# Optimization experiments

Measured on AMD Instinct MI355X. Metric: run time of the kernel, lower is better.

## Reference

```python
import jax, jax.numpy as jnp
import numpy as np
from jax import lax

H, H2, VJ, VC = 512, 256, 70, 2000
B, LIN, T = 64, 1024, 256
START = 1  # char2index['<s>']


def gru_step(h, x, Wih, Whh, bih, bhh):
    # PyTorch GRU cell math; gates ordered (r, z, n)
    gi = x @ Wih.T + bih
    gh = h @ Whh.T + bhh
    ir, iz, inn = jnp.split(gi, 3, axis=-1)
    hr, hz, hn = jnp.split(gh, 3, axis=-1)
    r = jax.nn.sigmoid(ir + hr)
    z = jax.nn.sigmoid(iz + hz)
    n = jnp.tanh(inn + r * hn)
    return (1.0 - z) * n + z * h


def setup_inputs() -> dict:
    key = jax.random.key(0)
    ks = jax.random.split(key, 24)
    u = lambda k, s: jax.random.uniform(k, s, jnp.float32, -0.1, 0.1)
    return {
        "input_tokens": jax.random.randint(ks[0], (B, LIN), 0, VJ),
        "target_tokens": jax.random.randint(ks[1], (B, T), 0, VC),
        "loss_mask": jnp.ones((B, T), jnp.float32),
        "emb_jamo": u(ks[2], (VJ, H)),
        "emb_char": u(ks[3], (VC, H)),
        "enc_Wih_f": u(ks[4], (3 * H2, H)),  "enc_Whh_f": u(ks[5], (3 * H2, H2)),
        "enc_bih_f": u(ks[6], (3 * H2,)),    "enc_bhh_f": u(ks[7], (3 * H2,)),
        "enc_Wih_b": u(ks[8], (3 * H2, H)),  "enc_Whh_b": u(ks[9], (3 * H2, H2)),
        "enc_bih_b": u(ks[10], (3 * H2,)),   "enc_bhh_b": u(ks[11], (3 * H2,)),
        "dec_Wih": u(ks[12], (3 * H, H)),    "dec_Whh": u(ks[13], (3 * H, H)),
        "dec_bih": u(ks[14], (3 * H,)),      "dec_bhh": u(ks[15], (3 * H,)),
        "attn_W": u(ks[16], (H, 2 * H)),     "attn_b": u(ks[17], (H,)),
        "comb_W": u(ks[18], (H, 2 * H)),     "comb_b": u(ks[19], (H,)),
        "out_W": u(ks[20], (VC, H)),         "out_b": u(ks[21], (VC,)),
    }


def reference(input_tokens, target_tokens, loss_mask, emb_jamo, emb_char,
              enc_Wih_f, enc_Whh_f, enc_bih_f, enc_bhh_f,
              enc_Wih_b, enc_Whh_b, enc_bih_b, enc_bhh_b,
              dec_Wih, dec_Whh, dec_bih, dec_bhh,
              attn_W, attn_b, comb_W, comb_b, out_W, out_b):
    b, lin = input_tokens.shape
    t_len = target_tokens.shape[1]
    h2 = enc_Whh_f.shape[1]

    # --- Encoder: step-by-step bidirectional GRU (per original Python loop,
    # both directions advance forward in time since seq_len=1 per call) ---
    xs = jnp.swapaxes(emb_jamo[input_tokens], 0, 1)  # [Lin, B, H]

    def enc_step(carry, xt):
        hf, hb = carry
        hf = gru_step(hf, xt, enc_Wih_f, enc_Whh_f, enc_bih_f, enc_bhh_f)
        hb = gru_step(hb, xt, enc_Wih_b, enc_Whh_b, enc_bih_b, enc_bhh_b)
        return (hf, hb), jnp.concatenate([hf, hb], axis=-1)

    init = (jnp.zeros((b, h2), xs.dtype), jnp.zeros((b, h2), xs.dtype))
    _, enc_out_t = lax.scan(enc_step, init, xs)      # [Lin, B, H]
    enc_out = jnp.swapaxes(enc_out_t, 0, 1)          # [B, Lin, H]
    h0 = enc_out_t[-1]                               # decoder init hidden [B, H]

    # --- Decoder: attention + GRU, greedy argmax feedback ---
    tok0 = jnp.full((b,), START, dtype=input_tokens.dtype)

    def dec_step(carry, _):
        tok, h = carry
        emb = emb_char[tok]                                           # [B, H]
        key_ = jnp.concatenate([emb, h], -1) @ attn_W.T + attn_b      # [B, H]
        scores = jnp.einsum('blh,bh->bl', enc_out, key_)              # [B, Lin]
        w = jax.nn.softmax(scores, axis=1)
        ctx = jnp.einsum('bl,blh->bh', w, enc_out)                    # [B, H]
        g = jax.nn.relu(jnp.concatenate([emb, ctx], -1) @ comb_W.T + comb_b)
        h_new = gru_step(h, g, dec_Wih, dec_Whh, dec_bih, dec_bhh)
        logp = jax.nn.log_softmax(h_new @ out_W.T + out_b, axis=-1)   # [B, VC]
        nxt = jnp.argmax(logp, axis=-1).astype(tok.dtype)
        return (nxt, h_new), (logp, w)

    _, (logps, ws) = lax.scan(dec_step, (tok0, h0), None, length=t_len)
    decoder_outputs = jnp.swapaxes(logps, 0, 1)       # [B, T, VC]
    decoder_attentions = jnp.transpose(ws, (1, 2, 0)) # [B, Lin, T]

    # NLLLoss(reduction='none') masked, mean over batch, summed over steps, /T
    nll = -jnp.take_along_axis(decoder_outputs, target_tokens[..., None], axis=-1)[..., 0]
    loss = jnp.sum(jnp.mean(nll * loss_mask, axis=0)) / t_len
    return decoder_outputs, decoder_attentions, loss
```

## Files before the change

kernel.cpp:

```cpp
#include <hip/hip_runtime.h>
#include <hip/hip_bf16.h>
#include <cstdint>
#include <cstddef>


#define DEV __device__ __forceinline__

constexpr int kH = 512, kH2 = 256, kVC = 2000, kB = 64, kLIN = 1024, kT = 256;
constexpr int kSTART = 1;

__global__ __launch_bounds__(256) void k_zero(float* p, int n) {
  int i = blockIdx.x * 256 + threadIdx.x;
  if (i < n) p[i] = 0.f;
}

__global__ __launch_bounds__(256)
void k_gi_table(const float* emb_jamo, const float* Wf, const float* Wb,
                const float* bihf, const float* bihb, float* gi) {
  int v = blockIdx.x >> 1, d = blockIdx.x & 1;
  const float* W = d ? Wb : Wf;
  const float* bih = d ? bihb : bihf;
  __shared__ float x[kH];
  for (int k = threadIdx.x; k < kH; k += 256) x[k] = emb_jamo[v * kH + k];
  __syncthreads();
  for (int j = threadIdx.x; j < 3 * kH2; j += 256) {
    float acc = bih[j];
    const float* row = W + (size_t)j * kH;
    for (int k = 0; k < kH; k += 4) {
      float4 f = *(const float4*)(row + k);
      acc += x[k] * f.x + x[k + 1] * f.y + x[k + 2] * f.z + x[k + 3] * f.w;
    }
    gi[(size_t)(v * 2 + d) * 768 + j] = acc;
  }
}

__global__ __launch_bounds__(256)
void k_ac_emb(const float* emb_char, const float* attn_W, const float* attn_b,
              const float* comb_W, const float* comb_b, float* A, float* C) {
  int v = blockIdx.x;
  __shared__ float x[kH];
  for (int k = threadIdx.x; k < kH; k += 256) x[k] = emb_char[v * kH + k];
  __syncthreads();
  for (int j = threadIdx.x; j < kH; j += 256) {
    float a = attn_b[j], c = comb_b[j];
    const float* ra = attn_W + (size_t)j * 1024;
    const float* rc = comb_W + (size_t)j * 1024;
    for (int k = 0; k < kH; k += 4) {
      float4 fa = *(const float4*)(ra + k), fc = *(const float4*)(rc + k);
      a += x[k] * fa.x + x[k + 1] * fa.y + x[k + 2] * fa.z + x[k + 3] * fa.w;
      c += x[k] * fc.x + x[k + 1] * fc.y + x[k + 2] * fc.z + x[k + 3] * fc.w;
    }
    A[(size_t)v * kH + j] = a;
    C[(size_t)v * kH + j] = c;
  }
}

__global__ __launch_bounds__(256)
void k_enc_step(const int* tokens, const float* Whf, const float* Whb,
                const float* bhhf, const float* bhhb, const float* gi,
                float* henc, float* enc, int t, int pp, int BC, int lbc, int b0) {
  int d = blockIdx.x >> lbc;
  int blk = blockIdx.x & (BC - 1);
  int b = threadIdx.x & (BC - 1), q = threadIdx.x >> lbc;
  int u = blk * (256 >> lbc) + q;
  const float* Whh = d ? Whb : Whf;
  const float* bhh = d ? bhhb : bhhf;
  const float* hin = henc + (size_t)(pp * 2 + d) * kH2 * BC;
  float* hout = henc + (size_t)((1 - pp) * 2 + d) * kH2 * BC;

  const float* wr = Whh + (size_t)(0 * kH2 + u) * kH2;
  const float* wz = Whh + (size_t)(1 * kH2 + u) * kH2;
  const float* wn = Whh + (size_t)(2 * kH2 + u) * kH2;
  float ar = bhh[u], az = bhh[kH2 + u], an = bhh[2 * kH2 + u];
  for (int k = 0; k < kH2; k += 4) {
    float4 fr = *(const float4*)(wr + k);
    float4 fz = *(const float4*)(wz + k);
    float4 fn = *(const float4*)(wn + k);
    float h0v = hin[(k + 0) * BC + b], h1v = hin[(k + 1) * BC + b];
    float h2v = hin[(k + 2) * BC + b], h3v = hin[(k + 3) * BC + b];
    ar += h0v * fr.x + h1v * fr.y + h2v * fr.z + h3v * fr.w;
    az += h0v * fz.x + h1v * fz.y + h2v * fz.z + h3v * fz.w;
    an += h0v * fn.x + h1v * fn.y + h2v * fn.z + h3v * fn.w;
  }
  int v = tokens[(size_t)(b0 + b) * kLIN + t];
  const float* git = gi + (size_t)(v * 2 + d) * 768;
  float r = 1.f / (1.f + expf(-(git[u] + ar)));
  float z = 1.f / (1.f + expf(-(git[kH2 + u] + az)));
  float n = tanhf(git[2 * kH2 + u] + r * an);
  float hprev = hin[u * BC + b];
  float hnew = (1.f - z) * n + z * hprev;
  hout[u * BC + b] = hnew;
  enc[((size_t)b * kLIN + t) * kH + d * kH2 + u] = hnew;
}

__global__ __launch_bounds__(256)
void k_prologue(const float* enc, const float* Atab, const float* aW,
                float* hr, float* ht, float* key, int* tok, int BC) {
  int b = blockIdx.x, tid = threadIdx.x;
  __shared__ float h[kH];
  const float* h0 = enc + ((size_t)b * kLIN + (kLIN - 1)) * kH;
  for (int k = tid; k < kH; k += 256) {
    float v = h0[k];
    h[k] = v;
    hr[(size_t)b * kH + k] = v;
    ht[(size_t)k * BC + b] = v;
  }
  if (tid == 0) tok[b] = kSTART;
  __syncthreads();
  const float* A = Atab + (size_t)kSTART * kH;
  for (int j = tid; j < kH; j += 256) {
    const float* row = aW + (size_t)j * 1024 + 512;
    float acc = A[j];
    for (int k = 0; k < kH; k += 4) {
      float4 f = *(const float4*)(row + k);
      acc += h[k] * f.x + h[k + 1] * f.y + h[k + 2] * f.z + h[k + 3] * f.w;
    }
    key[(size_t)b * kH + j] = acc;
  }
}

__global__ __launch_bounds__(256)
void k_scores(const float* encAll, const float* keyAll, float* sc,
              float* pm, float* pd, float* pctx) {
  int b = blockIdx.x >> 3, lt = blockIdx.x & 7;
  int tid = threadIdx.x, lane = tid & 63, w = tid >> 6, hl = lane & 31, half = lane >> 5;
  __shared__ float s_tile[128], e_tile[128], red[128];
  const float* enc = encAll + (size_t)b * kLIN * kH;
  float kreg[16];
  const float* key = keyAll + (size_t)b * kH + hl * 16;
#pragma unroll
  for (int m = 0; m < 16; m += 4) *(float4*)(kreg + m) = *(const float4*)(key + m);
  for (int i = 0; i < 16; i++) {
    int ll = w * 32 + i * 2 + half;
    int l = lt * 128 + ll;
    const float* row = enc + (size_t)l * kH + hl * 16;
    float acc = 0.f;
#pragma unroll
    for (int m = 0; m < 16; m += 4) {
      float4 v = *(const float4*)(row + m);
      acc += v.x * kreg[m] + v.y * kreg[m + 1] + v.z * kreg[m + 2] + v.w * kreg[m + 3];
    }
#pragma unroll
    for (int m2 = 16; m2 > 0; m2 >>= 1) acc += __shfl_xor(acc, m2, 32);
    if (hl == 0) { s_tile[ll] = acc; sc[(size_t)b * kLIN + l] = acc; }
  }
  __syncthreads();
  if (tid < 128) red[tid] = s_tile[tid];
  __syncthreads();
  for (int s = 64; s > 0; s >>= 1) {
    if (tid < s) red[tid] = fmaxf(red[tid], red[tid + s]);
    __syncthreads();
  }
  float mt = red[0];
  __syncthreads();
  if (tid < 128) { e_tile[tid] = expf(s_tile[tid] - mt); red[tid] = e_tile[tid]; }
  __syncthreads();
  for (int s = 64; s > 0; s >>= 1) {
    if (tid < s) red[tid] += red[tid + s];
    __syncthreads();
  }
  float dt = red[0];
  int h0i = tid * 2;
  float cx = 0.f, cy = 0.f;
  const float* base = enc + (size_t)(lt * 128) * kH + h0i;
  for (int l = 0; l < 128; l++) {
    float e = e_tile[l];
    float2 v = *(const float2*)(base + (size_t)l * kH);
    cx += e * v.x; cy += e * v.y;
  }
  float* pc = pctx + ((size_t)b * 8 + lt) * kH;
  pc[h0i] = cx; pc[h0i + 1] = cy;
  if (tid == 0) { pm[b * 8 + lt] = mt; pd[b * 8 + lt] = dt; }
}

__global__ __launch_bounds__(256)
void k_ctx_g(const float* cW, const float* Ctab, const float* sc,
             const float* pm, const float* pd, const float* pctx,
             const int* tok, float* out1, float* gt, int BC, int b0, int t) {
  int b = blockIdx.x, tid = threadIdx.x;
  __shared__ float f8[8], MD[2], ctxl[kH];
  __shared__ int tokl;
  if (tid == 0) {
    float M = -1e30f;
    for (int i = 0; i < 8; i++) M = fmaxf(M, pm[b * 8 + i]);
    float D = 0.f;
    for (int i = 0; i < 8; i++) {
      float f = expf(pm[b * 8 + i] - M);
      f8[i] = f; D += f * pd[b * 8 + i];
    }
    MD[0] = M; MD[1] = 1.f / D;
    tokl = tok[b];
  }
  __syncthreads();
  float M = MD[0], invD = MD[1];
  int h0i = tid * 2;
  float cx = 0.f, cy = 0.f;
  for (int i = 0; i < 8; i++) {
    const float* pc = pctx + ((size_t)b * 8 + i) * kH + h0i;
    cx += f8[i] * pc[0]; cy += f8[i] * pc[1];
  }
  ctxl[h0i] = cx * invD; ctxl[h0i + 1] = cy * invD;
  int gb = b0 + b;
  for (int l = tid; l < kLIN; l += 256)
    out1[((size_t)gb * kLIN + l) * kT + t] = expf(sc[(size_t)b * kLIN + l] - M) * invD;
  __syncthreads();
  int tk = tokl;
  for (int j = tid; j < kH; j += 256) {
    const float* row = cW + (size_t)j * 1024 + 512;
    float acc = Ctab[(size_t)tk * kH + j];
    for (int k = 0; k < kH; k += 4) {
      float4 f = *(const float4*)(row + k);
      acc += ctxl[k] * f.x + ctxl[k + 1] * f.y + ctxl[k + 2] * f.z + ctxl[k + 3] * f.w;
    }
    gt[(size_t)j * BC + b] = fmaxf(acc, 0.f);
  }
}

__global__ __launch_bounds__(256)
void k_gru(const float* Wih, const float* Whh, const float* bih, const float* bhh,
           const float* gt, float* ht, float* hr, int BC, int lbc, int pp) {
  int tid = threadIdx.x;
  int b = tid & (BC - 1), q = tid >> lbc;
  int u = blockIdx.x * (256 >> lbc) + q;
  const float* htp = ht + (size_t)pp * kH * BC;
  float air = bih[u], aiz = bih[kH + u], ain = bih[2 * kH + u];
  float ahr = bhh[u], ahz = bhh[kH + u], ahn = bhh[2 * kH + u];
  const float* wir = Wih + (size_t)(0 * kH + u) * kH;
  const float* wiz = Wih + (size_t)(1 * kH + u) * kH;
  const float* win = Wih + (size_t)(2 * kH + u) * kH;
  const float* whr = Whh + (size_t)(0 * kH + u) * kH;
  const float* whz = Whh + (size_t)(1 * kH + u) * kH;
  const float* whn = Whh + (size_t)(2 * kH + u) * kH;
  for (int k = 0; k < kH; k += 4) {
    float4 fir = *(const float4*)(wir + k), fiz = *(const float4*)(wiz + k), fin = *(const float4*)(win + k);
    float4 fhr = *(const float4*)(whr + k), fhz = *(const float4*)(whz + k), fhn = *(const float4*)(whn + k);
    float g0 = gt[(k + 0) * BC + b], g1 = gt[(k + 1) * BC + b];
    float g2 = gt[(k + 2) * BC + b], g3 = gt[(k + 3) * BC + b];
    float h0v = htp[(k + 0) * BC + b], h1v = htp[(k + 1) * BC + b];
    float h2v = htp[(k + 2) * BC + b], h3v = htp[(k + 3) * BC + b];
    air += g0 * fir.x + g1 * fir.y + g2 * fir.z + g3 * fir.w;
    aiz += g0 * fiz.x + g1 * fiz.y + g2 * fiz.z + g3 * fiz.w;
    ain += g0 * fin.x + g1 * fin.y + g2 * fin.z + g3 * fin.w;
    ahr += h0v * fhr.x + h1v * fhr.y + h2v * fhr.z + h3v * fhr.w;
    ahz += h0v * fhz.x + h1v * fhz.y + h2v * fhz.z + h3v * fhz.w;
    ahn += h0v * fhn.x + h1v * fhn.y + h2v * fhn.z + h3v * fhn.w;
  }
  float r = 1.f / (1.f + expf(-(air + ahr)));
  float z = 1.f / (1.f + expf(-(aiz + ahz)));
  float n = tanhf(ain + r * ahn);
  float hp = htp[(size_t)u * BC + b];
  float hnew = (1.f - z) * n + z * hp;
  ht[(size_t)(1 - pp) * kH * BC + (size_t)u * BC + b] = hnew;
  hr[(size_t)(1 - pp) * BC * kH + (size_t)b * kH + u] = hnew;
}

__global__ __launch_bounds__(256)
void k_logits(const float* oW, const float* ob, const float* hr, float* lg,
              int BC, int np) {
  int b = blockIdx.x >> 3, ct = blockIdx.x & 7;
  int tid = threadIdx.x, lane = tid & 63, w = tid >> 6, hl = lane & 31, half = lane >> 5;
  const float* hrow = hr + (size_t)np * BC * kH + (size_t)b * kH + hl * 16;
  float hreg[16];
#pragma unroll
  for (int m = 0; m < 16; m += 4) *(float4*)(hreg + m) = *(const float4*)(hrow + m);
  int c0 = ct * 250;
  for (int i = 0; i < 32; i++) {
    int c = c0 + i * 8 + w * 2 + half;
    if (c < c0 + 250) {
      const float* row = oW + (size_t)c * kH + hl * 16;
      float acc = 0.f;
#pragma unroll
      for (int m = 0; m < 16; m += 4) {
        float4 v = *(const float4*)(row + m);
        acc += v.x * hreg[m] + v.y * hreg[m + 1] + v.z * hreg[m + 2] + v.w * hreg[m + 3];
      }
#pragma unroll
      for (int m2 = 16; m2 > 0; m2 >>= 1) acc += __shfl_xor(acc, m2, 32);
      if (hl == 0) lg[(size_t)b * kVC + c] = acc + ob[c];
    }
  }
}

__global__ __launch_bounds__(256)
void k_finish(const float* aW, const int* targets, const float* mask,
              const float* Atab, const float* hr, const float* lg,
              float* key, int* tok, float* loss, float* out0,
              int BC, int b0, int t, int np) {
  int b = blockIdx.x, tid = threadIdx.x, gb = b0 + b;
  __shared__ float rv[256]; __shared__ int ri[256]; __shared__ float rs[256];
  __shared__ float hsh[kH];
  const float* lrow = lg + (size_t)b * kVC;
  float xv[8];
  float bv = -3.4e38f; int bi = kVC;
#pragma unroll
  for (int i = 0; i < 8; i++) {
    int c = tid + i * 256;
    float x = (c < kVC) ? lrow[c] : -3.4e38f;
    xv[i] = x;
    if (x > bv) { bv = x; bi = c; }
  }
  rv[tid] = bv; ri[tid] = bi;
  __syncthreads();
  for (int s = 128; s > 0; s >>= 1) {
    if (tid < s) {
      float v2 = rv[tid + s]; int i2 = ri[tid + s];
      if (v2 > rv[tid] || (v2 == rv[tid] && i2 < ri[tid])) { rv[tid] = v2; ri[tid] = i2; }
    }
    __syncthreads();
  }
  float M = rv[0]; int nt = ri[0];
  float se = 0.f;
#pragma unroll
  for (int i = 0; i < 8; i++) { int c = tid + i * 256; if (c < kVC) se += expf(xv[i] - M); }
  rs[tid] = se;
  __syncthreads();
  for (int s = 128; s > 0; s >>= 1) {
    if (tid < s) rs[tid] += rs[tid + s];
    __syncthreads();
  }
  float lse = M + logf(rs[0]);
  float* orow = out0 + ((size_t)gb * kT + t) * kVC;
#pragma unroll
  for (int i = 0; i < 8; i++) { int c = tid + i * 256; if (c < kVC) orow[c] = xv[i] - lse; }
  if (tid == 0) {
    tok[b] = nt;
    int tg = targets[(size_t)gb * kT + t];
    float mk = mask[(size_t)gb * kT + t];
    atomicAdd(loss, (lse - lrow[tg]) * mk * (1.f / 16384.f));
  }
  const float* hrow = hr + (size_t)np * BC * kH + (size_t)b * kH;
  for (int k = tid; k < kH; k += 256) hsh[k] = hrow[k];
  __syncthreads();
  const float* A = Atab + (size_t)nt * kH;
  for (int j = tid; j < kH; j += 256) {
    const float* row = aW + (size_t)j * 1024 + 512;
    float acc = A[j];
    for (int k = 0; k < kH; k += 4) {
      float4 f = *(const float4*)(row + k);
      acc += hsh[k] * f.x + hsh[k + 1] * f.y + hsh[k + 2] * f.z + hsh[k + 3] * f.w;
    }
    key[(size_t)b * kH + j] = acc;
  }
}

__global__ void k_loss_out(float* dst, const float* loss) {
  if (threadIdx.x == 0 && blockIdx.x == 0) *dst = *loss;
}

extern "C" void kernel_launch(void* const* d_in, const int* in_sizes, int n_in,
                              void* d_out, int out_size, void* d_ws, size_t ws_size,
                              hipStream_t stream) {
  (void)in_sizes; (void)n_in;
  const int*   tok_in = (const int*)d_in[0];
  const int*   tgt    = (const int*)d_in[1];
  const float* mask   = (const float*)d_in[2];
  const float* emb_j  = (const float*)d_in[3];
  const float* emb_c  = (const float*)d_in[4];
  const float* eWif   = (const float*)d_in[5];
  const float* eWhf   = (const float*)d_in[6];
  const float* ebif   = (const float*)d_in[7];
  const float* ebhf   = (const float*)d_in[8];
  const float* eWib   = (const float*)d_in[9];
  const float* eWhb   = (const float*)d_in[10];
  const float* ebib   = (const float*)d_in[11];
  const float* ebhb   = (const float*)d_in[12];
  const float* dWi    = (const float*)d_in[13];
  const float* dWh    = (const float*)d_in[14];
  const float* dbi    = (const float*)d_in[15];
  const float* dbh    = (const float*)d_in[16];
  const float* aW     = (const float*)d_in[17];
  const float* ab     = (const float*)d_in[18];
  const float* cW     = (const float*)d_in[19];
  const float* cb     = (const float*)d_in[20];
  const float* oW     = (const float*)d_in[21];
  const float* ob     = (const float*)d_in[22];
  float* ws   = (float*)d_ws;
  float* out0 = (float*)d_out;
  float* out1 = out0 + (size_t)kB * kT * kVC;

  const size_t GI = 0;
  const size_t A  = GI + 107520;
  const size_t C  = A + 1024000;
  const size_t SMALL = C + 1024000;
  size_t o = SMALL;
  const size_t HENC = o; o += 4 * 256 * 64;
  const size_t KEY  = o; o += 64 * 512;
  const size_t SC   = o; o += 64 * 1024;
  const size_t PM   = o; o += 512;
  const size_t PD   = o; o += 512;
  const size_t PCT  = o; o += 64 * 8 * 512;
  const size_t GT   = o; o += 512 * 64;
  const size_t HR   = o; o += 2 * 64 * 512;
  const size_t HT   = o; o += 2 * 512 * 64;
  const size_t LG   = o; o += 64 * 2000;
  const size_t TOKo = o; o += 64;
  const size_t LOSS = o; o += 1;
  const size_t ENC  = o;
  const int small_n = (int)(ENC - SMALL);

  int BC = 64;
  while (BC > 8 && (ENC + (size_t)BC * kLIN * kH) * sizeof(float) > ws_size) BC >>= 1;
  int lbc = (BC == 64) ? 6 : (BC == 32) ? 5 : (BC == 16) ? 4 : 3;
  int NC = kB / BC;
  int* tokp = (int*)(ws + TOKo);

  k_zero<<<(small_n + 255) / 256, 256, 0, stream>>>(ws + SMALL, small_n);
  k_gi_table<<<140, 256, 0, stream>>>(emb_j, eWif, eWib, ebif, ebib, ws + GI);
  k_ac_emb<<<2000, 256, 0, stream>>>(emb_c, aW, ab, cW, cb, ws + A, ws + C);

  for (int c = 0; c < NC; c++) {
    int b0 = c * BC;
    k_zero<<<(4 * 256 * BC + 255) / 256, 256, 0, stream>>>(ws + HENC, 4 * 256 * BC);
    for (int t = 0; t < kLIN; t++)
      k_enc_step<<<2 * BC, 256, 0, stream>>>(tok_in, eWhf, eWhb, ebhf, ebhb,
                                             ws + GI, ws + HENC, ws + ENC,
                                             t, t & 1, BC, lbc, b0);
    k_prologue<<<BC, 256, 0, stream>>>(ws + ENC, ws + A, aW, ws + HR, ws + HT,
                                       ws + KEY, tokp, BC);
    for (int t = 0; t < kT; t++) {
      int pp = t & 1, np = 1 - pp;
      k_scores<<<BC * 8, 256, 0, stream>>>(ws + ENC, ws + KEY, ws + SC,
                                           ws + PM, ws + PD, ws + PCT);
      k_ctx_g<<<BC, 256, 0, stream>>>(cW, ws + C, ws + SC, ws + PM, ws + PD,
                                      ws + PCT, tokp, out1, ws + GT, BC, b0, t);
      k_gru<<<2 * BC, 256, 0, stream>>>(dWi, dWh, dbi, dbh, ws + GT,
                                        ws + HT, ws + HR, BC, lbc, pp);
      k_logits<<<BC * 8, 256, 0, stream>>>(oW, ob, ws + HR, ws + LG, BC, np);
      k_finish<<<BC, 256, 0, stream>>>(aW, tgt, mask, ws + A, ws + HR, ws + LG,
                                       ws + KEY, tokp, ws + LOSS, out0,
                                       BC, b0, t, np);
    }
  }
  k_loss_out<<<1, 64, 0, stream>>>(out0 + (size_t)out_size - 1, ws + LOSS);
}
```

Before: 62.72 ms.

## Replace per-step kernel launches with cooperative persistent encoder and decoder kernels

The encoder's 1024 per-timestep launches become one cooperative kernel that loops over time with grid.sync, caching each block's recurrent weight slice in LDS. The decoder's five launches per step are fused into one persistent cooperative kernel whose phases are separated by grid-wide barriers. The aim is to remove kernel launch overhead and weight reloads across thousands of tiny sequential launches. In exchange it relies on grid barrier cost and cooperative-launch support, and keeps the old launch sequence as a fallback if that launch fails.

```diff
diff --git a/kernel.cpp b/kernel.cpp
--- a/kernel.cpp
+++ b/kernel.cpp
@@ -1,10 +1,10 @@
 #include <hip/hip_runtime.h>
-#include <hip/hip_bf16.h>
+#include <hip/hip_cooperative_groups.h>
 #include <cstdint>
 #include <cstddef>
 
-
-#define DEV __device__ __forceinline__
+namespace cg = cooperative_groups;
+
 
 constexpr int kH = 512, kH2 = 256, kVC = 2000, kB = 64, kLIN = 1024, kT = 256;
 constexpr int kSTART = 1;
@@ -55,75 +55,11 @@
   }
 }
 
-__global__ __launch_bounds__(256)
-void k_enc_step(const int* tokens, const float* Whf, const float* Whb,
-                const float* bhhf, const float* bhhb, const float* gi,
-                float* henc, float* enc, int t, int pp, int BC, int lbc, int b0) {
-  int d = blockIdx.x >> lbc;
-  int blk = blockIdx.x & (BC - 1);
-  int b = threadIdx.x & (BC - 1), q = threadIdx.x >> lbc;
-  int u = blk * (256 >> lbc) + q;
-  const float* Whh = d ? Whb : Whf;
-  const float* bhh = d ? bhhb : bhhf;
-  const float* hin = henc + (size_t)(pp * 2 + d) * kH2 * BC;
-  float* hout = henc + (size_t)((1 - pp) * 2 + d) * kH2 * BC;
-
-  const float* wr = Whh + (size_t)(0 * kH2 + u) * kH2;
-  const float* wz = Whh + (size_t)(1 * kH2 + u) * kH2;
-  const float* wn = Whh + (size_t)(2 * kH2 + u) * kH2;
-  float ar = bhh[u], az = bhh[kH2 + u], an = bhh[2 * kH2 + u];
-  for (int k = 0; k < kH2; k += 4) {
-    float4 fr = *(const float4*)(wr + k);
-    float4 fz = *(const float4*)(wz + k);
-    float4 fn = *(const float4*)(wn + k);
-    float h0v = hin[(k + 0) * BC + b], h1v = hin[(k + 1) * BC + b];
-    float h2v = hin[(k + 2) * BC + b], h3v = hin[(k + 3) * BC + b];
-    ar += h0v * fr.x + h1v * fr.y + h2v * fr.z + h3v * fr.w;
-    az += h0v * fz.x + h1v * fz.y + h2v * fz.z + h3v * fz.w;
-    an += h0v * fn.x + h1v * fn.y + h2v * fn.z + h3v * fn.w;
-  }
-  int v = tokens[(size_t)(b0 + b) * kLIN + t];
-  const float* git = gi + (size_t)(v * 2 + d) * 768;
-  float r = 1.f / (1.f + expf(-(git[u] + ar)));
-  float z = 1.f / (1.f + expf(-(git[kH2 + u] + az)));
-  float n = tanhf(git[2 * kH2 + u] + r * an);
-  float hprev = hin[u * BC + b];
-  float hnew = (1.f - z) * n + z * hprev;
-  hout[u * BC + b] = hnew;
-  enc[((size_t)b * kLIN + t) * kH + d * kH2 + u] = hnew;
-}
-
-__global__ __launch_bounds__(256)
-void k_prologue(const float* enc, const float* Atab, const float* aW,
-                float* hr, float* ht, float* key, int* tok, int BC) {
-  int b = blockIdx.x, tid = threadIdx.x;
-  __shared__ float h[kH];
-  const float* h0 = enc + ((size_t)b * kLIN + (kLIN - 1)) * kH;
-  for (int k = tid; k < kH; k += 256) {
-    float v = h0[k];
-    h[k] = v;
-    hr[(size_t)b * kH + k] = v;
-    ht[(size_t)k * BC + b] = v;
-  }
-  if (tid == 0) tok[b] = kSTART;
-  __syncthreads();
-  const float* A = Atab + (size_t)kSTART * kH;
-  for (int j = tid; j < kH; j += 256) {
-    const float* row = aW + (size_t)j * 1024 + 512;
-    float acc = A[j];
-    for (int k = 0; k < kH; k += 4) {
-      float4 f = *(const float4*)(row + k);
-      acc += h[k] * f.x + h[k + 1] * f.y + h[k + 2] * f.z + h[k + 3] * f.w;
-    }
-    key[(size_t)b * kH + j] = acc;
-  }
-}
-
-__global__ __launch_bounds__(256)
-void k_scores(const float* encAll, const float* keyAll, float* sc,
-              float* pm, float* pd, float* pctx) {
-  int b = blockIdx.x >> 3, lt = blockIdx.x & 7;
-  int tid = threadIdx.x, lane = tid & 63, w = tid >> 6, hl = lane & 31, half = lane >> 5;
+
+__device__ void phaseA(int b, int lt, int tid, const float* encAll,
+                       const float* keyAll, float* sc, float* pm, float* pd,
+                       float* pctx) {
+  int lane = tid & 63, w = tid >> 6, hl = lane & 31, half = lane >> 5;
   __shared__ float s_tile[128], e_tile[128], red[128];
   const float* enc = encAll + (size_t)b * kLIN * kH;
   float kreg[16];
@@ -171,13 +107,13 @@
   float* pc = pctx + ((size_t)b * 8 + lt) * kH;
   pc[h0i] = cx; pc[h0i + 1] = cy;
   if (tid == 0) { pm[b * 8 + lt] = mt; pd[b * 8 + lt] = dt; }
-}
-
-__global__ __launch_bounds__(256)
-void k_ctx_g(const float* cW, const float* Ctab, const float* sc,
-             const float* pm, const float* pd, const float* pctx,
-             const int* tok, float* out1, float* gt, int BC, int b0, int t) {
-  int b = blockIdx.x, tid = threadIdx.x;
+  __syncthreads();
+}
+
+__device__ void phaseB(int b, int tid, const float* cW, const float* Ctab,
+                       const float* sc, const float* pm, const float* pd,
+                       const float* pctx, const int* tok, float* out1,
+                       float* gt, int BC, int b0, int t) {
   __shared__ float f8[8], MD[2], ctxl[kH];
   __shared__ int tokl;
   if (tid == 0) {
@@ -214,14 +150,14 @@
     }
     gt[(size_t)j * BC + b] = fmaxf(acc, 0.f);
   }
-}
-
-__global__ __launch_bounds__(256)
-void k_gru(const float* Wih, const float* Whh, const float* bih, const float* bhh,
-           const float* gt, float* ht, float* hr, int BC, int lbc, int pp) {
-  int tid = threadIdx.x;
+  __syncthreads();
+}
+
+__device__ void phaseC(int blk, int tid, const float* Wih, const float* Whh,
+                       const float* bih, const float* bhh, const float* gt,
+                       float* ht, float* hr, int BC, int lbc, int pp) {
   int b = tid & (BC - 1), q = tid >> lbc;
-  int u = blockIdx.x * (256 >> lbc) + q;
+  int u = blk * (256 >> lbc) + q;
   const float* htp = ht + (size_t)pp * kH * BC;
   float air = bih[u], aiz = bih[kH + u], ain = bih[2 * kH + u];
   float ahr = bhh[u], ahz = bhh[kH + u], ahn = bhh[2 * kH + u];
@@ -254,11 +190,9 @@
   hr[(size_t)(1 - pp) * BC * kH + (size_t)b * kH + u] = hnew;
 }
 
-__global__ __launch_bounds__(256)
-void k_logits(const float* oW, const float* ob, const float* hr, float* lg,
-              int BC, int np) {
-  int b = blockIdx.x >> 3, ct = blockIdx.x & 7;
-  int tid = threadIdx.x, lane = tid & 63, w = tid >> 6, hl = lane & 31, half = lane >> 5;
+__device__ void phaseD(int b, int ct, int tid, const float* oW, const float* ob,
+                       const float* hr, float* lg, int BC, int np) {
+  int lane = tid & 63, w = tid >> 6, hl = lane & 31, half = lane >> 5;
   const float* hrow = hr + (size_t)np * BC * kH + (size_t)b * kH + hl * 16;
   float hreg[16];
 #pragma unroll
@@ -281,12 +215,11 @@
   }
 }
 
-__global__ __launch_bounds__(256)
-void k_finish(const float* aW, const int* targets, const float* mask,
-              const float* Atab, const float* hr, const float* lg,
-              float* key, int* tok, float* loss, float* out0,
-              int BC, int b0, int t, int np) {
-  int b = blockIdx.x, tid = threadIdx.x, gb = b0 + b;
+__device__ void phaseE(int b, int tid, const float* aW, const int* targets,
+                       const float* mask, const float* Atab, const float* hr,
+                       const float* lg, float* key, int* tok, float* loss,
+                       float* out0, int BC, int b0, int t, int np) {
+  int gb = b0 + b;
   __shared__ float rv[256]; __shared__ int ri[256]; __shared__ float rs[256];
   __shared__ float hsh[kH];
   const float* lrow = lg + (size_t)b * kVC;
@@ -341,11 +274,211 @@
     }
     key[(size_t)b * kH + j] = acc;
   }
+  __syncthreads();
+}
+
+
+__global__ __launch_bounds__(256, 1)
+void k_enc_persist(const int* tokens, const float* Whf, const float* Whb,
+                   const float* bhhf, const float* bhhb, const float* gi,
+                   float* henc, float* enc, int BC, int lbc, int b0) {
+  cg::grid_group grid = cg::this_grid();
+  extern __shared__ float wlds[];
+  int d = blockIdx.x >> lbc;
+  int blk = blockIdx.x & (BC - 1);
+  int b = threadIdx.x & (BC - 1), q = threadIdx.x >> lbc;
+  int nu = 256 >> lbc;
+  int u = blk * nu + q;
+  const float* Whh = d ? Whb : Whf;
+  const float* bhh = d ? bhhb : bhhf;
+  bool useLds = ((size_t)3 * nu * kH2 * 4 <= 48 * 1024);
+  const float *wr, *wz, *wn;
+  if (useLds) {
+    int q4 = kH2 / 4;
+    int tot4 = 3 * nu * q4;
+    for (int i4 = threadIdx.x; i4 < tot4; i4 += 256) {
+      int r = i4 / q4;
+      int k4 = i4 - r * q4;
+      int g = r / nu, qq = r - g * nu;
+      *(float4*)(wlds + (size_t)r * kH2 + k4 * 4) =
+          *(const float4*)(Whh + (size_t)(g * kH2 + blk * nu + qq) * kH2 + k4 * 4);
+    }
+    __syncthreads();
+    wr = wlds + (size_t)(0 * nu + q) * kH2;
+    wz = wlds + (size_t)(1 * nu + q) * kH2;
+    wn = wlds + (size_t)(2 * nu + q) * kH2;
+  } else {
+    wr = Whh + (size_t)(0 * kH2 + u) * kH2;
+    wz = Whh + (size_t)(1 * kH2 + u) * kH2;
+    wn = Whh + (size_t)(2 * kH2 + u) * kH2;
+  }
+  float br = bhh[u], bz = bhh[kH2 + u], bn = bhh[2 * kH2 + u];
+  const int* myTok = tokens + (size_t)(b0 + b) * kLIN;
+  for (int t = 0; t < kLIN; ++t) {
+    int pp = t & 1;
+    const float* hin = henc + (size_t)(pp * 2 + d) * kH2 * BC;
+    float* hout = henc + (size_t)((1 - pp) * 2 + d) * kH2 * BC;
+    float ar = br, az = bz, an = bn;
+    for (int k = 0; k < kH2; k += 4) {
+      float4 fr = *(const float4*)(wr + k);
+      float4 fz = *(const float4*)(wz + k);
+      float4 fn = *(const float4*)(wn + k);
+      float h0v = hin[(k + 0) * BC + b], h1v = hin[(k + 1) * BC + b];
+      float h2v = hin[(k + 2) * BC + b], h3v = hin[(k + 3) * BC + b];
+      ar += h0v * fr.x + h1v * fr.y + h2v * fr.z + h3v * fr.w;
+      az += h0v * fz.x + h1v * fz.y + h2v * fz.z + h3v * fz.w;
+      an += h0v * fn.x + h1v * fn.y + h2v * fn.z + h3v * fn.w;
+    }
+    int v = myTok[t];
+    const float* git = gi + (size_t)(v * 2 + d) * 768;
+    float r = 1.f / (1.f + expf(-(git[u] + ar)));
+    float z = 1.f / (1.f + expf(-(git[kH2 + u] + az)));
+    float n = tanhf(git[2 * kH2 + u] + r * an);
+    float hprev = hin[(size_t)u * BC + b];
+    float hnew = (1.f - z) * n + z * hprev;
+    hout[(size_t)u * BC + b] = hnew;
+    enc[((size_t)b * kLIN + t) * kH + d * kH2 + u] = hnew;
+    grid.sync();
+  }
+}
+
+__global__ __launch_bounds__(256, 2)
+void k_dec_persist(const float* encAll, const float* cW, const float* Ctab,
+                   const float* dWi, const float* dWh, const float* dbi, const float* dbh,
+                   const float* oW, const float* ob, const float* aW, const float* Atab,
+                   const int* targets, const float* mask,
+                   float* key, float* sc, float* pm, float* pd, float* pctx,
+                   float* gt, float* ht, float* hr, float* lg,
+                   int* tok, float* loss, float* out0, float* out1,
+                   int BC, int lbc, int b0) {
+  cg::grid_group grid = cg::this_grid();
+  int tid = threadIdx.x;
+  int G = gridDim.x;
+  for (int t = 0; t < kT; ++t) {
+    int pp = t & 1, np = 1 - pp;
+    for (int wk = blockIdx.x; wk < BC * 8; wk += G)
+      phaseA(wk >> 3, wk & 7, tid, encAll, key, sc, pm, pd, pctx);
+    grid.sync();
+    for (int wk = blockIdx.x; wk < BC; wk += G)
+      phaseB(wk, tid, cW, Ctab, sc, pm, pd, pctx, tok, out1, gt, BC, b0, t);
+    grid.sync();
+    for (int wk = blockIdx.x; wk < 2 * BC; wk += G)
+      phaseC(wk, tid, dWi, dWh, dbi, dbh, gt, ht, hr, BC, lbc, pp);
+    grid.sync();
+    for (int wk = blockIdx.x; wk < BC * 8; wk += G)
+      phaseD(wk >> 3, wk & 7, tid, oW, ob, hr, lg, BC, np);
+    grid.sync();
+    for (int wk = blockIdx.x; wk < BC; wk += G)
+      phaseE(wk, tid, aW, targets, mask, Atab, hr, lg, key, tok, loss,
+             out0, BC, b0, t, np);
+    grid.sync();
+  }
+}
+
+
+__global__ __launch_bounds__(256)
+void k_enc_step(const int* tokens, const float* Whf, const float* Whb,
+                const float* bhhf, const float* bhhb, const float* gi,
+                float* henc, float* enc, int t, int pp, int BC, int lbc, int b0) {
+  int d = blockIdx.x >> lbc;
+  int blk = blockIdx.x & (BC - 1);
+  int b = threadIdx.x & (BC - 1), q = threadIdx.x >> lbc;
+  int u = blk * (256 >> lbc) + q;
+  const float* Whh = d ? Whb : Whf;
+  const float* bhh = d ? bhhb : bhhf;
+  const float* hin = henc + (size_t)(pp * 2 + d) * kH2 * BC;
+  float* hout = henc + (size_t)((1 - pp) * 2 + d) * kH2 * BC;
+  const float* wr = Whh + (size_t)(0 * kH2 + u) * kH2;
+  const float* wz = Whh + (size_t)(1 * kH2 + u) * kH2;
+  const float* wn = Whh + (size_t)(2 * kH2 + u) * kH2;
+  float ar = bhh[u], az = bhh[kH2 + u], an = bhh[2 * kH2 + u];
+  for (int k = 0; k < kH2; k += 4) {
+    float4 fr = *(const float4*)(wr + k);
+    float4 fz = *(const float4*)(wz + k);
+    float4 fn = *(const float4*)(wn + k);
+    float h0v = hin[(k + 0) * BC + b], h1v = hin[(k + 1) * BC + b];
+    float h2v = hin[(k + 2) * BC + b], h3v = hin[(k + 3) * BC + b];
+    ar += h0v * fr.x + h1v * fr.y + h2v * fr.z + h3v * fr.w;
+    az += h0v * fz.x + h1v * fz.y + h2v * fz.z + h3v * fz.w;
+    an += h0v * fn.x + h1v * fn.y + h2v * fn.z + h3v * fn.w;
+  }
+  int v = tokens[(size_t)(b0 + b) * kLIN + t];
+  const float* git = gi + (size_t)(v * 2 + d) * 768;
+  float r = 1.f / (1.f + expf(-(git[u] + ar)));
+  float z = 1.f / (1.f + expf(-(git[kH2 + u] + az)));
+  float n = tanhf(git[2 * kH2 + u] + r * an);
+  float hprev = hin[(size_t)u * BC + b];
+  float hnew = (1.f - z) * n + z * hprev;
+  hout[(size_t)u * BC + b] = hnew;
+  enc[((size_t)b * kLIN + t) * kH + d * kH2 + u] = hnew;
+}
+
+__global__ __launch_bounds__(256)
+void k_scores(const float* encAll, const float* keyAll, float* sc,
+              float* pm, float* pd, float* pctx) {
+  phaseA(blockIdx.x >> 3, blockIdx.x & 7, threadIdx.x, encAll, keyAll, sc, pm, pd, pctx);
+}
+
+__global__ __launch_bounds__(256)
+void k_ctx_g(const float* cW, const float* Ctab, const float* sc,
+             const float* pm, const float* pd, const float* pctx,
+             const int* tok, float* out1, float* gt, int BC, int b0, int t) {
+  phaseB(blockIdx.x, threadIdx.x, cW, Ctab, sc, pm, pd, pctx, tok, out1, gt, BC, b0, t);
+}
+
+__global__ __launch_bounds__(256)
+void k_gru(const float* Wih, const float* Whh, const float* bih, const float* bhh,
+           const float* gt, float* ht, float* hr, int BC, int lbc, int pp) {
+  phaseC(blockIdx.x, threadIdx.x, Wih, Whh, bih, bhh, gt, ht, hr, BC, lbc, pp);
+}
+
+__global__ __launch_bounds__(256)
+void k_logits(const float* oW, const float* ob, const float* hr, float* lg,
+              int BC, int np) {
+  phaseD(blockIdx.x >> 3, blockIdx.x & 7, threadIdx.x, oW, ob, hr, lg, BC, np);
+}
+
+__global__ __launch_bounds__(256)
+void k_finish(const float* aW, const int* targets, const float* mask,
+              const float* Atab, const float* hr, const float* lg,
+              float* key, int* tok, float* loss, float* out0,
+              int BC, int b0, int t, int np) {
+  phaseE(blockIdx.x, threadIdx.x, aW, targets, mask, Atab, hr, lg, key, tok,
+         loss, out0, BC, b0, t, np);
+}
+
+__global__ __launch_bounds__(256)
+void k_prologue(const float* enc, const float* Atab, const float* aW,
+                float* hr, float* ht, float* key, int* tok, int BC) {
+  int b = blockIdx.x, tid = threadIdx.x;
+  __shared__ float h[kH];
+  const float* h0 = enc + ((size_t)b * kLIN + (kLIN - 1)) * kH;
+  for (int k = tid; k < kH; k += 256) {
+    float v = h0[k];
+    h[k] = v;
+    hr[(size_t)b * kH + k] = v;
+    ht[(size_t)k * BC + b] = v;
+  }
+  if (tid == 0) tok[b] = kSTART;
+  __syncthreads();
+  const float* A = Atab + (size_t)kSTART * kH;
+  for (int j = tid; j < kH; j += 256) {
+    const float* row = aW + (size_t)j * 1024 + 512;
+    float acc = A[j];
+    for (int k = 0; k < kH; k += 4) {
+      float4 f = *(const float4*)(row + k);
+      acc += h[k] * f.x + h[k + 1] * f.y + h[k + 2] * f.z + h[k + 3] * f.w;
+    }
+    key[(size_t)b * kH + j] = acc;
+  }
 }
 
 __global__ void k_loss_out(float* dst, const float* loss) {
   if (threadIdx.x == 0 && blockIdx.x == 0) *dst = *loss;
 }
+
+static int g_coop = -1;
+static int g_dec_grid = 0;
 
 extern "C" void kernel_launch(void* const* d_in, const int* in_sizes, int n_in,
                               void* d_out, int out_size, void* d_ws, size_t ws_size,
@@ -402,34 +535,97 @@
   while (BC > 8 && (ENC + (size_t)BC * kLIN * kH) * sizeof(float) > ws_size) BC >>= 1;
   int lbc = (BC == 64) ? 6 : (BC == 32) ? 5 : (BC == 16) ? 4 : 3;
   int NC = kB / BC;
+  int nu = 256 >> lbc;
+  size_t wbytes = (size_t)3 * nu * kH2 * 4;
+  unsigned enc_smem = (wbytes <= 48 * 1024) ? (unsigned)wbytes : 0u;
+
+  float* gi_p   = ws + GI;
+  float* A_p    = ws + A;
+  float* C_p    = ws + C;
+  float* henc_p = ws + HENC;
+  float* key_p  = ws + KEY;
+  float* sc_p   = ws + SC;
+  float* pm_p   = ws + PM;
+  float* pd_p   = ws + PD;
+  float* pct_p  = ws + PCT;
+  float* gt_p   = ws + GT;
+  float* hr_p   = ws + HR;
+  float* ht_p   = ws + HT;
+  float* lg_p   = ws + LG;
+  float* loss_p = ws + LOSS;
+  float* enc_p  = ws + ENC;
   int* tokp = (int*)(ws + TOKo);
 
+  if (g_dec_grid == 0) {
+    int ma = 0;
+    hipError_t oe = hipOccupancyMaxActiveBlocksPerMultiprocessor(
+        &ma, reinterpret_cast<const void*>(&k_dec_persist), 256, (size_t)0);
+    if (oe != hipSuccess || ma < 1) { ma = 1; (void)hipGetLastError(); }
+    long g = (long)ma * 256;
+    if (g > 512) g = 512;
+    g_dec_grid = (int)g;
+  }
+  int decGrid = g_dec_grid;
+  if (decGrid > BC * 8) decGrid = BC * 8;
+
   k_zero<<<(small_n + 255) / 256, 256, 0, stream>>>(ws + SMALL, small_n);
-  k_gi_table<<<140, 256, 0, stream>>>(emb_j, eWif, eWib, ebif, ebib, ws + GI);
-  k_ac_emb<<<2000, 256, 0, stream>>>(emb_c, aW, ab, cW, cb, ws + A, ws + C);
+  k_gi_table<<<140, 256, 0, stream>>>(emb_j, eWif, eWib, ebif, ebib, gi_p);
+  k_ac_emb<<<2000, 256, 0, stream>>>(emb_c, aW, ab, cW, cb, A_p, C_p);
 
   for (int c = 0; c < NC; c++) {
     int b0 = c * BC;
-    k_zero<<<(4 * 256 * BC + 255) / 256, 256, 0, stream>>>(ws + HENC, 4 * 256 * BC);
-    for (int t = 0; t < kLIN; t++)
-      k_enc_step<<<2 * BC, 256, 0, stream>>>(tok_in, eWhf, eWhb, ebhf, ebhb,
-                                             ws + GI, ws + HENC, ws + ENC,
-                                             t, t & 1, BC, lbc, b0);
-    k_prologue<<<BC, 256, 0, stream>>>(ws + ENC, ws + A, aW, ws + HR, ws + HT,
-                                       ws + KEY, tokp, BC);
-    for (int t = 0; t < kT; t++) {
-      int pp = t & 1, np = 1 - pp;
-      k_scores<<<BC * 8, 256, 0, stream>>>(ws + ENC, ws + KEY, ws + SC,
-                                           ws + PM, ws + PD, ws + PCT);
-      k_ctx_g<<<BC, 256, 0, stream>>>(cW, ws + C, ws + SC, ws + PM, ws + PD,
-                                      ws + PCT, tokp, out1, ws + GT, BC, b0, t);
-      k_gru<<<2 * BC, 256, 0, stream>>>(dWi, dWh, dbi, dbh, ws + GT,
-                                        ws + HT, ws + HR, BC, lbc, pp);
-      k_logits<<<BC * 8, 256, 0, stream>>>(oW, ob, ws + HR, ws + LG, BC, np);
-      k_finish<<<BC, 256, 0, stream>>>(aW, tgt, mask, ws + A, ws + HR, ws + LG,
-                                       ws + KEY, tokp, ws + LOSS, out0,
-                                       BC, b0, t, np);
-    }
-  }
-  k_loss_out<<<1, 64, 0, stream>>>(out0 + (size_t)out_size - 1, ws + LOSS);
-}
+    k_zero<<<(4 * 256 * BC + 255) / 256, 256, 0, stream>>>(henc_p, 4 * 256 * BC);
+
+    bool enc_done = false;
+    if (g_coop != 0) {
+      void* eargs[] = {(void*)&tok_in, (void*)&eWhf, (void*)&eWhb, (void*)&ebhf,
+                       (void*)&ebhb, (void*)&gi_p, (void*)&henc_p, (void*)&enc_p,
+                       (void*)&BC, (void*)&lbc, (void*)&b0};
+      hipError_t e = hipLaunchCooperativeKernel(
+          reinterpret_cast<void*>(k_enc_persist), dim3(2 * BC), dim3(256),
+          eargs, enc_smem, stream);
+      if (e == hipSuccess) { enc_done = true; if (g_coop < 0) g_coop = 1; }
+      else { g_coop = 0; (void)hipGetLastError(); }
+    }
+    if (!enc_done) {
+      for (int t = 0; t < kLIN; t++)
+        k_enc_step<<<2 * BC, 256, 0, stream>>>(tok_in, eWhf, eWhb, ebhf, ebhb,
+                                               gi_p, henc_p, enc_p,
+                                               t, t & 1, BC, lbc, b0);
+    }
+
+    k_prologue<<<BC, 256, 0, stream>>>(enc_p, A_p, aW, hr_p, ht_p, key_p, tokp, BC);
+
+    bool dec_done = false;
+    if (g_coop != 0) {
+      void* dargs[] = {(void*)&enc_p, (void*)&cW, (void*)&C_p, (void*)&dWi,
+                       (void*)&dWh, (void*)&dbi, (void*)&dbh, (void*)&oW,
+                       (void*)&ob, (void*)&aW, (void*)&A_p, (void*)&tgt,
+                       (void*)&mask, (void*)&key_p, (void*)&sc_p, (void*)&pm_p,
+                       (void*)&pd_p, (void*)&pct_p, (void*)&gt_p, (void*)&ht_p,
+                       (void*)&hr_p, (void*)&lg_p, (void*)&tokp, (void*)&loss_p,
+                       (void*)&out0, (void*)&out1, (void*)&BC, (void*)&lbc,
+                       (void*)&b0};
+      hipError_t e = hipLaunchCooperativeKernel(
+          reinterpret_cast<void*>(k_dec_persist), dim3(decGrid), dim3(256),
+          dargs, 0, stream);
+      if (e == hipSuccess) { dec_done = true; if (g_coop < 0) g_coop = 1; }
+      else { g_coop = 0; (void)hipGetLastError(); }
+    }
+    if (!dec_done) {
+      for (int t = 0; t < kT; t++) {
+        int pp = t & 1, np = 1 - pp;
+        k_scores<<<BC * 8, 256, 0, stream>>>(enc_p, key_p, sc_p, pm_p, pd_p, pct_p);
+        k_ctx_g<<<BC, 256, 0, stream>>>(cW, C_p, sc_p, pm_p, pd_p, pct_p,
+                                        tokp, out1, gt_p, BC, b0, t);
+        k_gru<<<2 * BC, 256, 0, stream>>>(dWi, dWh, dbi, dbh, gt_p,
+                                          ht_p, hr_p, BC, lbc, pp);
+        k_logits<<<BC * 8, 256, 0, stream>>>(oW, ob, hr_p, lg_p, BC, np);
+        k_finish<<<BC, 256, 0, stream>>>(aW, tgt, mask, A_p, hr_p, lg_p,
+                                         key_p, tokp, loss_p, out0,
+                                         BC, b0, t, np);
+      }
+    }
+  }
+  k_loss_out<<<1, 64, 0, stream>>>(out0 + (size_t)out_size - 1, loss_p);
+}
```

Measured after the change: 135.6 ms. +116.1%, slower.
